# Optimization experiments

Hardware: AMD Instinct MI355X
Metric: run time of the kernel (lower is better)

The kernel has to match this reference:

```python
import jax, jax.numpy as jnp
import numpy as np

WEIGHT = 1000.0      # start/end cell penalty
LONELY_W = 15.0      # cell lit outside cluster
CLUSTER_W = 5.0      # cell unlit inside cluster
CELL_W = 20.0        # cell on a shortest manhattan path
CSIZE_W = 12.0       # cluster-size penalty
GAP_W = 300.0        # gap-to-endpoint penalty
H = W = 10


def _md(y1, x1, y2, x2):
    return jnp.abs(y1 - y2) + jnp.abs(x1 - x2)


def _per_sample(result, points):
    # result: [H, W] float, points: [2, 2] int (row, col) of start and end
    p0y, p0x = points[0, 0], points[0, 1]
    p1y, p1x = points[1, 0], points[1, 1]
    base = _md(p0y, p0x, p1y, p1x)

    loss_start = (2.0 - (result[p0y, p0x] + result[p1y, p1x])) * WEIGHT

    # 8-connected flood fill from start over cells whose value rounds to 1.
    mask = jnp.round(result) == 1.0
    seed = jnp.zeros((H, W), bool).at[p0y, p0x].set(True)

    def dilate(_, c):
        p = jnp.pad(c, 1)
        nb = (p[:-2, :-2] | p[:-2, 1:-1] | p[:-2, 2:] |
              p[1:-1, :-2] | p[1:-1, 2:] |
              p[2:, :-2] | p[2:, 1:-1] | p[2:, 2:])
        return c | (nb & mask)

    # 8-connected diameter of a 10x10 grid is 9; H+W iterations is a safe bound.
    cluster = jax.lax.fori_loop(0, H + W, dilate, seed)

    rows = jnp.arange(H)[:, None]
    cols = jnp.arange(W)[None, :]

    # per-cell manhattan detour penalty
    d2 = _md(rows, cols, p0y, p0x) + _md(rows, cols, p1y, p1x)
    delta = (d2 - base).astype(result.dtype)
    single_cell = jnp.sum(jnp.where(delta == 0.0,
                                    (1.0 - result) * CELL_W,
                                    result * delta * 0.5))

    # NB: the original tests [column, row] membership against [row, col]
    # cluster entries -> transposed membership map. Faithfully reproduced.
    in_cl = cluster.T
    csize = jnp.sum(cluster).astype(result.dtype)
    lonelyness = jnp.sum(jnp.where(in_cl, (1.0 - result) * CLUSTER_W,
                                   result * LONELY_W))
    cluster_size_pen = jnp.sum(jnp.where(in_cl, result * csize * CSIZE_W, 0.0))

    # nearest cluster cell to the end point (strict improvement over base)
    dist_end = _md(rows, cols, p1y, p1x)
    masked = jnp.where(cluster, dist_end, H * W + 10).reshape(-1)
    idx = jnp.argmin(masked)
    minval = masked[idx]
    better = minval < base
    ny = jnp.where(better, idx // W, p0y)
    nx = jnp.where(better, idx % W, p0x)
    gap = jnp.minimum(base, minval)

    oy = p1y - ny
    ox = p1x - nx

    def upd(cond, cy, cx, st):
        by, bx, bg = st
        d = _md(cy, cx, p1y, p1x)
        b = cond & (d < bg)
        return (jnp.where(b, cy, by), jnp.where(b, cx, bx), jnp.where(b, d, bg))

    st = (ny, nx, gap)
    c = ox < 0
    st = upd(c, ny, nx - 1, st)
    st = upd(c & (ny != 0), ny - 1, nx - 1, st)
    st = upd(c & (ny != H - 1), ny + 1, nx - 1, st)
    c = ox > 0
    st = upd(c, ny, nx + 1, st)
    st = upd(c & (ny != 0), ny - 1, nx + 1, st)
    st = upd(c & (ny != H - 1), ny + 1, nx + 1, st)
    st = upd(oy < 0, ny - 1, nx, st)
    st = upd(oy > 0, ny + 1, nx, st)
    ncy = jnp.clip(st[0], 0, H - 1)
    ncx = jnp.clip(st[1], 0, W - 1)

    gap_pen = gap.astype(result.dtype) * GAP_W * (1.0 - result[ncy, ncx])

    return loss_start + lonelyness + single_cell + cluster_size_pen + gap_pen


def setup_inputs() -> dict:
    key = jax.random.key(0)
    k1, k2 = jax.random.split(key)
    B = 262144
    result_given = jax.random.uniform(k1, (B, 1, H, W), dtype=jnp.float32)
    points_given = jax.random.randint(k2, (B, 2, 2), 0, 10, dtype=jnp.int64 if jax.config.jax_enable_x64 else jnp.int32)
    return {"result_given": result_given, "points_given": points_given}


def reference(result_given, points_given):
    losses = jax.vmap(_per_sample)(result_given[:, 0], points_given)
    return jnp.sum(losses).reshape(1)
```

## Files before the change

kernel.cpp:

```cpp
#include <hip/hip_runtime.h>
#include <cstdint>

#define GH 10
#define GW 10

__global__ __launch_bounds__(256, 6) void custom_loss_kernel(
    const float* __restrict__ result,
    const int* __restrict__ points,
    float* __restrict__ out,
    int B)
{
    const int tid = blockIdx.x * blockDim.x + threadIdx.x;
    const int s = tid >> 1;
    const int h = tid & 1;
    float loss = 0.f;
    if (s < B) {
        const float* __restrict__ r = result + (size_t)s * 100;
        const int4 p = ((const int4*)points)[s];
        const int p0y = p.x, p0x = p.y, p1y = p.z, p1x = p.w;
        const int dy0 = abs(p0y - p1y), dx0 = abs(p0x - p1x);
        const int base = dy0 + dx0;
        const int idx0 = p0y * GW + p0x;
        const int idx1 = p1y * GW + p1x;
        const float rs = r[idx0];
        const float re = r[idx1];

        float adxf[10];
        uint32_t inbox_m = 0;
#pragma unroll
        for (int x = 0; x < 10; ++x) {
            const int a = abs(x - p0x) + abs(x - p1x) - dx0;
            adxf[x] = (float)a;
            inbox_m |= (a == 0) ? (1u << x) : 0u;
        }

        const int ybase = 5 * h;
        const float* __restrict__ rh = r + ybase * 10;
        float sum_h = 0.f, sc_h = 0.f, box_h = 0.f;
        uint64_t mword = 0;
#pragma unroll
        for (int i = 0; i < 5; ++i) {
            const int y = ybase + i;
            const float4 a4 = *(const float4*)(rh + i * 10);
            const float4 b4 = *(const float4*)(rh + i * 10 + 4);
            const float2 c2 = *(const float2*)(rh + i * 10 + 8);
            const float vv[10] = {a4.x, a4.y, a4.z, a4.w,
                                  b4.x, b4.y, b4.z, b4.w, c2.x, c2.y};
            const float rowacc = ((vv[0]+vv[1])+(vv[2]+vv[3])) +
                                 ((vv[4]+vv[5])+(vv[6]+vv[7])) + (vv[8]+vv[9]);
            sum_h += rowacc;
            const int ay = abs(y - p0y) + abs(y - p1y) - dy0;
            sc_h = fmaf((float)ay, rowacc, sc_h);
            float boxrow = 0.f;
            uint32_t rm = 0u;
#pragma unroll
            for (int x = 0; x < 10; ++x) {
                const float xv = vv[x];
                sc_h = fmaf(adxf[x], xv, sc_h);
                boxrow += ((inbox_m >> x) & 1u) ? xv : 0.f;
                rm |= (xv > 0.5f) ? (1u << x) : 0u;
            }
            box_h += (ay == 0) ? boxrow : 0.f;
            mword |= (uint64_t)rm << (10 * i);
        }
        const float sum_all = sum_h + __shfl_xor(sum_h, 1);
        const float sc      = sc_h  + __shfl_xor(sc_h, 1);
        const float boxSum  = box_h + __shfl_xor(box_h, 1);

        const uint64_t M50 = (1ull << 50) - 1;
        const uint64_t C0  = 0x10040100401ull;
        const uint64_t NC0 = M50 & ~C0;
        const uint64_t NC9 = M50 & ~(C0 << 9);
        uint64_t c = 0;
        if (h == 0) { if (idx0 <  50) c = 1ull << idx0; }
        else        { if (idx0 >= 50) c = 1ull << (idx0 - 50); }
#pragma unroll 1
        for (int it = 0; it < GH + GW; ++it) {
            const uint64_t ho = c | ((c << 1) & NC0) | ((c >> 1) & NC9);
            const uint64_t hother =
                (uint64_t)__shfl_xor((unsigned long long)ho, 1);
            const uint64_t inc = h ? (hother >> 40) : ((hother & 0x3FFull) << 40);
            const uint64_t n = ((ho | (ho << 10) | (ho >> 10) | inc) & mword) | c;
            int ch = (n != c);
            ch |= __shfl_xor(ch, 1);
            c = n;
            if (!ch) break;
        }
        const int Kh = __popcll(c);
        const int K = Kh + __shfl_xor(Kh, 1);

        const uint64_t c_other = (uint64_t)__shfl_xor((unsigned long long)c, 1);
        const uint64_t clo = h ? c_other : c;
        const uint64_t chi = h ? c : c_other;

        const uint64_t wlo = clo >> (5 * h);
        const uint64_t whi = chi >> (5 * h);
        float st_h = 0.f;
#pragma unroll
        for (int i = 0; i < 5; ++i) {
            const float4 a4 = *(const float4*)(rh + i * 10);
            const float4 b4 = *(const float4*)(rh + i * 10 + 4);
            const float2 c2 = *(const float2*)(rh + i * 10 + 8);
            const float vv[10] = {a4.x, a4.y, a4.z, a4.w,
                                  b4.x, b4.y, b4.z, b4.w, c2.x, c2.y};
#pragma unroll
            for (int x = 0; x < 10; ++x) {
                const uint64_t w = (x < 5) ? wlo : whi;
                const uint32_t bit = (uint32_t)((w >> ((x % 5) * 10 + i)) & 1ull);
                st_h = fmaf((float)bit, vv[x], st_h);
            }
        }
        const float S_T = st_h + __shfl_xor(st_h, 1);

        int bestd = 1000, bidx = 0;
#pragma unroll
        for (int i = 0; i < 5; ++i) {
            const int y = ybase + i;
            const uint32_t rb = (uint32_t)((c >> (10 * i)) & 0x3FFull);
            const uint32_t left  = rb & ((2u << p1x) - 1);
            const uint32_t right = rb >> p1x;
            const int dl = left  ? (p1x - (31 - __builtin_clz(left))) : 1000;
            const int dr = right ? __builtin_ctz(right) : 1000;
            int dx, xx;
            if (dl <= dr) { dx = dl; xx = p1x - dl; }
            else          { dx = dr; xx = p1x + dr; }
            const int d = abs(y - p1y) + dx;
            if (rb && d < bestd) { bestd = d; bidx = y * GW + xx; }
        }
        {
            const int od = __shfl_xor(bestd, 1);
            const int oi = __shfl_xor(bidx, 1);
            if (od < bestd || (od == bestd && oi < bidx)) { bestd = od; bidx = oi; }
        }

        if (h == 0) {
            const bool better = bestd < base;
            const int ny = better ? bidx / 10 : p0y;
            const int nx = better ? bidx % 10 : p0x;
            const int gap = min(base, bestd);

            int by = ny, bx = nx, bg = gap;
            const int oy = p1y - ny, ox = p1x - nx;
            auto upd = [&](bool cond, int cy, int cx) {
                const int d = abs(cy - p1y) + abs(cx - p1x);
                if (cond && (d < bg)) { by = cy; bx = cx; bg = d; }
            };
            upd(ox < 0,                     ny,     nx - 1);
            upd((ox < 0) && (ny != 0),      ny - 1, nx - 1);
            upd((ox < 0) && (ny != GH - 1), ny + 1, nx - 1);
            upd(ox > 0,                     ny,     nx + 1);
            upd((ox > 0) && (ny != 0),      ny - 1, nx + 1);
            upd((ox > 0) && (ny != GH - 1), ny + 1, nx + 1);
            upd(oy < 0,                     ny - 1, nx);
            upd(oy > 0,                     ny + 1, nx);
            const int ncy = min(max(by, 0), GH - 1);
            const int ncx = min(max(bx, 0), GW - 1);
            const float rn = r[ncy * GW + ncx];

            const float csf = (float)K;
            const float nboxf = (float)((dy0 + 1) * (dx0 + 1));
            const float loss_start = (2.f - (rs + re)) * 1000.f;
            const float lon = 5.f * csf + 15.f * sum_all - 20.f * S_T;
            const float single_cell = 0.5f * sc + 20.f * (nboxf - boxSum);
            const float cpen = 12.f * csf * S_T;
            const float gap_pen = (float)gap * 300.f * (1.f - rn);
            loss = loss_start + lon + single_cell + cpen + gap_pen;
        }
    }

#pragma unroll
    for (int off = 32; off > 0; off >>= 1)
        loss += __shfl_down(loss, off);
    __shared__ float wsum[4];
    const int lane = threadIdx.x & 63;
    const int wid = threadIdx.x >> 6;
    if (lane == 0) wsum[wid] = loss;
    __syncthreads();
    if (threadIdx.x == 0)
        atomicAdd(out, wsum[0] + wsum[1] + wsum[2] + wsum[3]);
}

extern "C" void kernel_launch(void* const* d_in, const int* in_sizes, int n_in,
                              void* d_out, int out_size, void* d_ws, size_t ws_size,
                              hipStream_t stream)
{
    const float* result = (const float*)d_in[0];
    const int* points   = (const int*)d_in[1];
    float* out = (float*)d_out;
    const int B = in_sizes[0] / 100;
    hipMemsetAsync(out, 0, sizeof(float), stream);
    const int block = 256;
    const int grid = (2 * B + block - 1) / block;
    custom_loss_kernel<<<grid, block, 0, stream>>>(result, points, out, B);
}
```

Baseline: 191.8 us.

## Stage block's samples in LDS with coalesced loads and run flood fill redundantly per lane

Each block first copies its 128 samples' grids into shared memory with coalesced float4 loads, then both half-threads read their 50 cells from LDS into registers once, so the second global pass over the grid goes away. The flood fill now runs on both 64-bit halves in every lane after exchanging the mask once, which removes the per-iteration cross-lane shuffles. The epilogue runs on both lanes instead of branching on h. This costs 51KB of LDS per block, which cuts occupancy (launch bounds lowered to 3), adds a block-wide barrier and doubles the flood-fill ALU work.

```diff
diff --git a/kernel.cpp b/kernel.cpp
--- a/kernel.cpp
+++ b/kernel.cpp
@@ -4,50 +4,69 @@
 #define GH 10
 #define GW 10
 
-__global__ __launch_bounds__(256, 6) void custom_loss_kernel(
+__global__ __launch_bounds__(256, 3) void custom_loss_kernel(
     const float* __restrict__ result,
     const int* __restrict__ points,
     float* __restrict__ out,
     int B)
 {
-    const int tid = blockIdx.x * blockDim.x + threadIdx.x;
-    const int s = tid >> 1;
-    const int h = tid & 1;
+    __shared__ float lds[128 * 100];
+    const int tix = threadIdx.x;
+
+    {
+        const size_t base4 = (size_t)blockIdx.x * (128 * 25);
+        const size_t total4 = (size_t)B * 25;
+        float4* lds4 = (float4*)lds;
+        const float4* g4 = (const float4*)result;
+#pragma unroll
+        for (int k = 0; k < 12; ++k) {
+            const int off = k * 256 + tix;
+            if (base4 + off < total4) lds4[off] = g4[base4 + off];
+        }
+        const int off = 12 * 256 + tix;
+        if (tix < 128 && base4 + off < total4) lds4[off] = g4[base4 + off];
+    }
+    __syncthreads();
+
+    const int s_local = tix >> 1;
+    const int h = tix & 1;
+    const int s = blockIdx.x * 128 + s_local;
     float loss = 0.f;
     if (s < B) {
-        const float* __restrict__ r = result + (size_t)s * 100;
+        const float* __restrict__ sp = lds + s_local * 100;
         const int4 p = ((const int4*)points)[s];
         const int p0y = p.x, p0x = p.y, p1y = p.z, p1x = p.w;
         const int dy0 = abs(p0y - p1y), dx0 = abs(p0x - p1x);
-        const int base = dy0 + dx0;
+        const int base0 = dy0 + dx0;
         const int idx0 = p0y * GW + p0x;
         const int idx1 = p1y * GW + p1x;
-        const float rs = r[idx0];
-        const float re = r[idx1];
-
-        float adxf[10];
-        uint32_t inbox_m = 0;
+        const float rs = sp[idx0];
+        const float re = sp[idx1];
+
+        float adxf[10], inboxf[10];
 #pragma unroll
         for (int x = 0; x < 10; ++x) {
             const int a = abs(x - p0x) + abs(x - p1x) - dx0;
             adxf[x] = (float)a;
-            inbox_m |= (a == 0) ? (1u << x) : 0u;
-        }
-
-        const int ybase = 5 * h;
-        const float* __restrict__ rh = r + ybase * 10;
+            inboxf[x] = (a == 0) ? 1.f : 0.f;
+        }
+
+        const float2* rp2 = (const float2*)(sp + h * 50);
+        float vv[50];
+#pragma unroll
+        for (int i = 0; i < 25; ++i) {
+            const float2 t = rp2[i];
+            vv[2 * i] = t.x; vv[2 * i + 1] = t.y;
+        }
+
         float sum_h = 0.f, sc_h = 0.f, box_h = 0.f;
         uint64_t mword = 0;
 #pragma unroll
         for (int i = 0; i < 5; ++i) {
-            const int y = ybase + i;
-            const float4 a4 = *(const float4*)(rh + i * 10);
-            const float4 b4 = *(const float4*)(rh + i * 10 + 4);
-            const float2 c2 = *(const float2*)(rh + i * 10 + 8);
-            const float vv[10] = {a4.x, a4.y, a4.z, a4.w,
-                                  b4.x, b4.y, b4.z, b4.w, c2.x, c2.y};
-            const float rowacc = ((vv[0]+vv[1])+(vv[2]+vv[3])) +
-                                 ((vv[4]+vv[5])+(vv[6]+vv[7])) + (vv[8]+vv[9]);
+            const int y = 5 * h + i;
+            const float* v = vv + 10 * i;
+            const float rowacc = ((v[0]+v[1])+(v[2]+v[3])) +
+                                 ((v[4]+v[5])+(v[6]+v[7])) + (v[8]+v[9]);
             sum_h += rowacc;
             const int ay = abs(y - p0y) + abs(y - p1y) - dy0;
             sc_h = fmaf((float)ay, rowacc, sc_h);
@@ -55,10 +74,9 @@
             uint32_t rm = 0u;
 #pragma unroll
             for (int x = 0; x < 10; ++x) {
-                const float xv = vv[x];
-                sc_h = fmaf(adxf[x], xv, sc_h);
-                boxrow += ((inbox_m >> x) & 1u) ? xv : 0.f;
-                rm |= (xv > 0.5f) ? (1u << x) : 0u;
+                sc_h = fmaf(adxf[x], v[x], sc_h);
+                boxrow = fmaf(inboxf[x], v[x], boxrow);
+                rm |= (v[x] > 0.5f) ? (1u << x) : 0u;
             }
             box_h += (ay == 0) ? boxrow : 0.f;
             mword |= (uint64_t)rm << (10 * i);
@@ -66,57 +84,49 @@
         const float sum_all = sum_h + __shfl_xor(sum_h, 1);
         const float sc      = sc_h  + __shfl_xor(sc_h, 1);
         const float boxSum  = box_h + __shfl_xor(box_h, 1);
+        const uint64_t mo = (uint64_t)__shfl_xor((unsigned long long)mword, 1);
+        const uint64_t mlo = h ? mo : mword;
+        const uint64_t mhi = h ? mword : mo;
 
         const uint64_t M50 = (1ull << 50) - 1;
         const uint64_t C0  = 0x10040100401ull;
         const uint64_t NC0 = M50 & ~C0;
         const uint64_t NC9 = M50 & ~(C0 << 9);
-        uint64_t c = 0;
-        if (h == 0) { if (idx0 <  50) c = 1ull << idx0; }
-        else        { if (idx0 >= 50) c = 1ull << (idx0 - 50); }
+        uint64_t clo = 0, chi = 0;
+        if (idx0 < 50) clo = 1ull << idx0; else chi = 1ull << (idx0 - 50);
 #pragma unroll 1
         for (int it = 0; it < GH + GW; ++it) {
-            const uint64_t ho = c | ((c << 1) & NC0) | ((c >> 1) & NC9);
-            const uint64_t hother =
-                (uint64_t)__shfl_xor((unsigned long long)ho, 1);
-            const uint64_t inc = h ? (hother >> 40) : ((hother & 0x3FFull) << 40);
-            const uint64_t n = ((ho | (ho << 10) | (ho >> 10) | inc) & mword) | c;
-            int ch = (n != c);
-            ch |= __shfl_xor(ch, 1);
-            c = n;
-            if (!ch) break;
-        }
-        const int Kh = __popcll(c);
-        const int K = Kh + __shfl_xor(Kh, 1);
-
-        const uint64_t c_other = (uint64_t)__shfl_xor((unsigned long long)c, 1);
-        const uint64_t clo = h ? c_other : c;
-        const uint64_t chi = h ? c : c_other;
+            const uint64_t hlo = clo | ((clo << 1) & NC0) | ((clo >> 1) & NC9);
+            const uint64_t hhi = chi | ((chi << 1) & NC0) | ((chi >> 1) & NC9);
+            uint64_t nlo = (hlo | (hlo << 10) | (hlo >> 10) | ((hhi & 0x3FFull) << 40)) & mlo;
+            uint64_t nhi = (hhi | (hhi << 10) | (hhi >> 10) | (hlo >> 40)) & mhi;
+            nlo |= clo; nhi |= chi;
+            if (nlo == clo && nhi == chi) break;
+            clo = nlo; chi = nhi;
+        }
+        const int K = __popcll(clo) + __popcll(chi);
 
         const uint64_t wlo = clo >> (5 * h);
         const uint64_t whi = chi >> (5 * h);
         float st_h = 0.f;
 #pragma unroll
         for (int i = 0; i < 5; ++i) {
-            const float4 a4 = *(const float4*)(rh + i * 10);
-            const float4 b4 = *(const float4*)(rh + i * 10 + 4);
-            const float2 c2 = *(const float2*)(rh + i * 10 + 8);
-            const float vv[10] = {a4.x, a4.y, a4.z, a4.w,
-                                  b4.x, b4.y, b4.z, b4.w, c2.x, c2.y};
+            const float* v = vv + 10 * i;
 #pragma unroll
             for (int x = 0; x < 10; ++x) {
                 const uint64_t w = (x < 5) ? wlo : whi;
                 const uint32_t bit = (uint32_t)((w >> ((x % 5) * 10 + i)) & 1ull);
-                st_h = fmaf((float)bit, vv[x], st_h);
+                st_h = fmaf((float)bit, v[x], st_h);
             }
         }
         const float S_T = st_h + __shfl_xor(st_h, 1);
 
         int bestd = 1000, bidx = 0;
+        const uint64_t cw = h ? chi : clo;
 #pragma unroll
         for (int i = 0; i < 5; ++i) {
-            const int y = ybase + i;
-            const uint32_t rb = (uint32_t)((c >> (10 * i)) & 0x3FFull);
+            const int y = 5 * h + i;
+            const uint32_t rb = (uint32_t)((cw >> (10 * i)) & 0x3FFull);
             const uint32_t left  = rb & ((2u << p1x) - 1);
             const uint32_t right = rb >> p1x;
             const int dl = left  ? (p1x - (31 - __builtin_clz(left))) : 1000;
@@ -133,39 +143,38 @@
             if (od < bestd || (od == bestd && oi < bidx)) { bestd = od; bidx = oi; }
         }
 
-        if (h == 0) {
-            const bool better = bestd < base;
-            const int ny = better ? bidx / 10 : p0y;
-            const int nx = better ? bidx % 10 : p0x;
-            const int gap = min(base, bestd);
-
-            int by = ny, bx = nx, bg = gap;
-            const int oy = p1y - ny, ox = p1x - nx;
-            auto upd = [&](bool cond, int cy, int cx) {
-                const int d = abs(cy - p1y) + abs(cx - p1x);
-                if (cond && (d < bg)) { by = cy; bx = cx; bg = d; }
-            };
-            upd(ox < 0,                     ny,     nx - 1);
-            upd((ox < 0) && (ny != 0),      ny - 1, nx - 1);
-            upd((ox < 0) && (ny != GH - 1), ny + 1, nx - 1);
-            upd(ox > 0,                     ny,     nx + 1);
-            upd((ox > 0) && (ny != 0),      ny - 1, nx + 1);
-            upd((ox > 0) && (ny != GH - 1), ny + 1, nx + 1);
-            upd(oy < 0,                     ny - 1, nx);
-            upd(oy > 0,                     ny + 1, nx);
-            const int ncy = min(max(by, 0), GH - 1);
-            const int ncx = min(max(bx, 0), GW - 1);
-            const float rn = r[ncy * GW + ncx];
-
-            const float csf = (float)K;
-            const float nboxf = (float)((dy0 + 1) * (dx0 + 1));
-            const float loss_start = (2.f - (rs + re)) * 1000.f;
-            const float lon = 5.f * csf + 15.f * sum_all - 20.f * S_T;
-            const float single_cell = 0.5f * sc + 20.f * (nboxf - boxSum);
-            const float cpen = 12.f * csf * S_T;
-            const float gap_pen = (float)gap * 300.f * (1.f - rn);
-            loss = loss_start + lon + single_cell + cpen + gap_pen;
-        }
+        const bool better = bestd < base0;
+        const int ny = better ? bidx / 10 : p0y;
+        const int nx = better ? bidx % 10 : p0x;
+        const int gap = min(base0, bestd);
+
+        int by = ny, bx = nx, bg = gap;
+        const int oy = p1y - ny, ox = p1x - nx;
+        auto upd = [&](bool cond, int cy, int cx) {
+            const int d = abs(cy - p1y) + abs(cx - p1x);
+            if (cond && (d < bg)) { by = cy; bx = cx; bg = d; }
+        };
+        upd(ox < 0,                     ny,     nx - 1);
+        upd((ox < 0) && (ny != 0),      ny - 1, nx - 1);
+        upd((ox < 0) && (ny != GH - 1), ny + 1, nx - 1);
+        upd(ox > 0,                     ny,     nx + 1);
+        upd((ox > 0) && (ny != 0),      ny - 1, nx + 1);
+        upd((ox > 0) && (ny != GH - 1), ny + 1, nx + 1);
+        upd(oy < 0,                     ny - 1, nx);
+        upd(oy > 0,                     ny + 1, nx);
+        const int ncy = min(max(by, 0), GH - 1);
+        const int ncx = min(max(bx, 0), GW - 1);
+        const float rn = sp[ncy * GW + ncx];
+
+        const float csf = (float)K;
+        const float nboxf = (float)((dy0 + 1) * (dx0 + 1));
+        const float loss_start = (2.f - (rs + re)) * 1000.f;
+        const float lon = 5.f * csf + 15.f * sum_all - 20.f * S_T;
+        const float single_cell = 0.5f * sc + 20.f * (nboxf - boxSum);
+        const float cpen = 12.f * csf * S_T;
+        const float gap_pen = (float)gap * 300.f * (1.f - rn);
+        loss = loss_start + lon + single_cell + cpen + gap_pen;
+        if (h != 0) loss = 0.f;
     }
 
 #pragma unroll
```

After: 180.2 us. 6.0% less time.
